# Kernel tuning notes

Hardware: AMD Instinct MI355X
Metric: run time of the kernel (lower is better)

The kernel has to match this reference:

```python
import jax, jax.numpy as jnp
import numpy as np

B, D, H, G = 16384, 512, 128, 18  # batch, input_dim, hidden_dim, num_genres

def setup_inputs() -> dict:
    key = jax.random.key(0)
    ks = jax.random.split(key, 12)
    s = lambda *sh: 1.0 / np.sqrt(sh[-2] if len(sh) > 1 else 1.0)
    item_features = jax.random.normal(ks[0], (B, D), dtype=jnp.float32)
    genre_vectors = jax.random.randint(ks[1], (B, G), 0, 2).astype(jnp.float32)  # multi-hot
    # stacked per-genre expert MLP params: D -> 2H -> H -> H
    W1 = jax.random.normal(ks[2], (G, D, 2 * H), dtype=jnp.float32) / np.sqrt(D)
    b1 = jnp.zeros((G, 2 * H), dtype=jnp.float32)
    W2 = jax.random.normal(ks[3], (G, 2 * H, H), dtype=jnp.float32) / np.sqrt(2 * H)
    b2 = jnp.zeros((G, H), dtype=jnp.float32)
    W3 = jax.random.normal(ks[4], (G, H, H), dtype=jnp.float32) / np.sqrt(H)
    b3 = jnp.zeros((G, H), dtype=jnp.float32)
    # genre attention: D -> G, softmax
    Wa = jax.random.normal(ks[5], (D, G), dtype=jnp.float32) / np.sqrt(D)
    ba = jnp.zeros((G,), dtype=jnp.float32)
    # aggregation: (D + H) -> D
    Wagg = jax.random.normal(ks[6], (D + H, D), dtype=jnp.float32) / np.sqrt(D + H)
    bagg = jnp.zeros((D,), dtype=jnp.float32)
    return dict(item_features=item_features, genre_vectors=genre_vectors,
                W1=W1, b1=b1, W2=W2, b2=b2, W3=W3, b3=b3,
                Wa=Wa, ba=ba, Wagg=Wagg, bagg=bagg)

def reference(item_features, genre_vectors, W1, b1, W2, b2, W3, b3, Wa, ba, Wagg, bagg):
    # genre attention weights [B, G]
    attn = jax.nn.softmax(item_features @ Wa + ba, axis=-1)
    # run every genre expert on every item (dense grouped GEMM), then mask.
    h1 = jax.nn.relu(jnp.einsum('bd,gdh->bgh', item_features, W1) + b1)   # [B,G,2H]
    h2 = jax.nn.relu(jnp.einsum('bgh,ghk->bgk', h1, W2) + b2)            # [B,G,H]
    h3 = jnp.einsum('bgk,gkm->bgm', h2, W3) + b3                          # [B,G,H]
    # per (item, genre) weight: attention * membership, zero where not a member
    w = jnp.where(genre_vectors > 0, attn * genre_vectors, 0.0)          # [B,G]
    refinements = jnp.einsum('bg,bgm->bm', w, h3)                         # [B,H]
    combined = jnp.concatenate([item_features, refinements], axis=-1)    # [B,D+H]
    return jax.nn.relu(combined @ Wagg + bagg)                            # [B,D]
```

## Files before the change

kernel.cpp:

```cpp
#include <hip/hip_runtime.h>

#define NB 16384
#define ND 512
#define NH 128
#define NHH 256
#define NG 18

typedef short s8v __attribute__((ext_vector_type(8)));
typedef __bf16 bf8v __attribute__((ext_vector_type(8)));
typedef float f16v __attribute__((ext_vector_type(16)));
typedef unsigned int u4v __attribute__((ext_vector_type(4)));

static __device__ __forceinline__ unsigned short f2bf(float f) {
  unsigned int u = __builtin_bit_cast(unsigned int, f);
  u += 0x7FFFu + ((u >> 16) & 1u);
  return (unsigned short)(u >> 16);
}

static __device__ __forceinline__ f16v mfma32(s8v a, s8v b, f16v c) {
  return __builtin_amdgcn_mfma_f32_32x32x16_bf16(
      __builtin_bit_cast(bf8v, a), __builtin_bit_cast(bf8v, b), c, 0, 0, 0);
}

static __device__ __forceinline__ f16v zf16() {
  f16v v;
#pragma unroll
  for (int i = 0; i < 16; ++i) v[i] = 0.f;
  return v;
}

__global__ __launch_bounds__(256) void k_pack(const float* __restrict__ in,
                                              unsigned short* __restrict__ out,
                                              int K, int N) {
  const int g = blockIdx.y;
  const int c = blockIdx.x * 256 + threadIdx.x;
  const int nk = K >> 4;
  const int l = c & 63;
  const int t = c >> 6;
  const int nt = t / nk;
  const int ks = t - nt * nk;
  const int k0 = (ks << 4) + ((l >> 5) << 3);
  const int col = (nt << 5) + (l & 31);
  const float* ip = in + (size_t)g * K * N + (size_t)k0 * N + col;
  u4v pk;
#pragma unroll
  for (int j = 0; j < 4; ++j) {
    float x0 = ip[(size_t)(2 * j) * N];
    float x1 = ip[(size_t)(2 * j + 1) * N];
    pk[j] = (unsigned)f2bf(x0) | ((unsigned)f2bf(x1) << 16);
  }
  *(u4v*)(out + (size_t)g * K * N + ((size_t)c << 3)) = pk;
}

__global__ __launch_bounds__(256) void k_wat(const float* __restrict__ wa,
                                             float* __restrict__ wat) {
  int tid = blockIdx.x * 256 + threadIdx.x;
  if (tid < NG * ND) {
    int g = tid >> 9, d = tid & (ND - 1);
    wat[tid] = wa[d * NG + g];
  }
}

__global__ __launch_bounds__(256) void k_attn(const float* __restrict__ X,
                                              const float* __restrict__ GV,
                                              const float* __restrict__ wat,
                                              const float* __restrict__ ba,
                                              float* __restrict__ w,
                                              unsigned short* __restrict__ xb) {
  __shared__ float wl[NG * ND];
  const int tid = threadIdx.x;
  for (int i = tid; i < NG * ND; i += 256) wl[i] = wat[i];
  __syncthreads();
  const int lane = tid & 63;
  const int row = (blockIdx.x << 2) + (tid >> 6);
  const float* xr = X + (size_t)row * ND + (lane << 3);
  float x[8];
  {
    float4 a = *(const float4*)xr;
    float4 b = *(const float4*)(xr + 4);
    x[0] = a.x; x[1] = a.y; x[2] = a.z; x[3] = a.w;
    x[4] = b.x; x[5] = b.y; x[6] = b.z; x[7] = b.w;
  }
  {
    u4v p;
#pragma unroll
    for (int j = 0; j < 4; ++j)
      p[j] = (unsigned)f2bf(x[2 * j]) | ((unsigned)f2bf(x[2 * j + 1]) << 16);
    *(u4v*)(xb + (size_t)row * ND + (lane << 3)) = p;
  }
  float lg[NG];
#pragma unroll
  for (int g = 0; g < NG; ++g) {
    const float* wr = wl + g * ND + (lane << 3);
    float s = 0.f;
#pragma unroll
    for (int j = 0; j < 8; ++j) s += x[j] * wr[j];
    lg[g] = s;
  }
#pragma unroll
  for (int off = 32; off > 0; off >>= 1) {
#pragma unroll
    for (int g = 0; g < NG; ++g) lg[g] += __shfl_xor(lg[g], off);
  }
  float m = -3.4e38f;
#pragma unroll
  for (int g = 0; g < NG; ++g) { lg[g] += ba[g]; m = fmaxf(m, lg[g]); }
  float s = 0.f;
#pragma unroll
  for (int g = 0; g < NG; ++g) { lg[g] = expf(lg[g] - m); s += lg[g]; }
  float inv = 1.f / s;
  if (lane < NG) {
    float gv = GV[(size_t)row * NG + lane];
    w[(size_t)row * NG + lane] = gv > 0.f ? lg[lane] * inv * gv : 0.f;
  }
}

__global__ __launch_bounds__(512, 2) void k_main(
    const unsigned short* __restrict__ xb,
    const float* __restrict__ wbg,
    const unsigned short* __restrict__ w1p,
    const unsigned short* __restrict__ w2p,
    const unsigned short* __restrict__ w3p,
    const unsigned short* __restrict__ w4p,
    const float* __restrict__ b1, const float* __restrict__ b2,
    const float* __restrict__ b3, const float* __restrict__ bagg,
    float* __restrict__ out) {
  __shared__ __align__(16) char smem[119808];
  char* const XT = smem;
  char* const H1 = smem + 65536;
  char* const H2 = smem + 98304;
  float* const WL = (float*)(smem + 114688);

  const int tid = threadIdx.x;
  const int row0 = blockIdx.x << 6;
  const int wid = tid >> 6, lane = tid & 63;
  const int l31 = lane & 31, lh = lane >> 5;

#pragma unroll
  for (int i = 0; i < 8; ++i) {
    int ck = (i << 9) + tid;
    int mt = ck >> 11, ks = (ck >> 6) & 31, l = ck & 63;
    int grow = row0 + (mt << 5) + (l & 31);
    int col8 = (ks << 1) + (l >> 5);
    *(u4v*)(XT + (ck << 4)) =
        *(const u4v*)(xb + ((size_t)grow << 9) + (col8 << 3));
  }
  for (int i = tid; i < 64 * NG; i += 512) {
    int r = i / NG, g = i - r * NG;
    WL[r * 20 + g] = wbg[(size_t)(row0 + r) * NG + g];
  }

  const int nt2 = wid & 3, mt2 = wid >> 2;
  const unsigned short* const bp1 = w1p + (wid << 14) + (lane << 3);
  const unsigned short* const bp2 = w2p + (nt2 << 13) + (lane << 3);
  const unsigned short* const bp3 = w3p + (nt2 << 12) + (lane << 3);
  const unsigned short* const bp4a = w4p + (size_t)wid * 20480 + (lane << 3);
  const unsigned short* const bp4b = w4p + (size_t)(wid + 8) * 20480 + (lane << 3);

  s8v bq[4];
#pragma unroll
  for (int i = 0; i < 4; ++i) bq[i] = *(const s8v*)(bp1 + (i << 9));

  f16v racc = zf16();
  __syncthreads();

  for (int g = 0; g < NG; ++g) {
    const unsigned short* const bp1g = bp1 + (size_t)g * 131072;
    f16v acc1[2][2];
    acc1[0][0] = zf16(); acc1[0][1] = zf16();
    acc1[1][0] = zf16(); acc1[1][1] = zf16();
#pragma unroll
    for (int ks = 0; ks < 32; ++ks) {
      s8v bn;
      const bool havenext = (ks < 28) || (g + 1 < NG);
      if (havenext) {
        size_t off = (ks < 28) ? (size_t)((ks + 4) << 9)
                               : (size_t)131072 + ((ks - 28) << 9);
        bn = *(const s8v*)(bp1g + off);
      }
      s8v a0 = *(const s8v*)(XT + (ks << 10) + (lane << 4));
      s8v a1 = *(const s8v*)(XT + 32768 + (ks << 10) + (lane << 4));
      acc1[0][ks & 1] = mfma32(a0, bq[ks & 3], acc1[0][ks & 1]);
      acc1[1][ks & 1] = mfma32(a1, bq[ks & 3], acc1[1][ks & 1]);
      if (havenext) bq[ks & 3] = bn;
    }
    {
      const float bv1 = b1[(g << 8) + (wid << 5) + l31];
      const int gcol = (wid << 5) + l31;
      const int cbase = ((gcol >> 4) << 10) + ((((gcol >> 3) & 1) << 5) << 4) +
                        ((gcol & 7) << 1);
#pragma unroll
      for (int mt = 0; mt < 2; ++mt)
#pragma unroll
        for (int r = 0; r < 16; ++r) {
          const int rl = (r & 3) + ((r >> 2) << 3) + (lh << 2);
          float v = fmaxf(acc1[mt][0][r] + acc1[mt][1][r] + bv1, 0.f);
          *(unsigned short*)(H1 + (mt << 14) + cbase + (rl << 4)) = f2bf(v);
        }
    }
    const unsigned short* const bp2g = bp2 + ((size_t)g << 15);
    s8v b2f[16];
#pragma unroll
    for (int ks = 0; ks < 16; ++ks) b2f[ks] = *(const s8v*)(bp2g + (ks << 9));
    const float bv2 = b2[(g << 7) + (nt2 << 5) + l31];
    __syncthreads();

    f16v acc2a = zf16(), acc2b = zf16();
#pragma unroll
    for (int ks = 0; ks < 16; ks += 2) {
      s8v a0 = *(const s8v*)(H1 + (mt2 << 14) + (ks << 10) + (lane << 4));
      s8v a1 = *(const s8v*)(H1 + (mt2 << 14) + ((ks + 1) << 10) + (lane << 4));
      acc2a = mfma32(a0, b2f[ks], acc2a);
      acc2b = mfma32(a1, b2f[ks + 1], acc2b);
    }
    {
      const int gcol = (nt2 << 5) + l31;
      const int cbase = ((gcol >> 4) << 10) + ((((gcol >> 3) & 1) << 5) << 4) +
                        ((gcol & 7) << 1);
#pragma unroll
      for (int r = 0; r < 16; ++r) {
        const int rl = (r & 3) + ((r >> 2) << 3) + (lh << 2);
        float v = fmaxf(acc2a[r] + acc2b[r] + bv2, 0.f);
        *(unsigned short*)(H2 + (mt2 << 13) + cbase + (rl << 4)) = f2bf(v);
      }
    }
    const unsigned short* const bp3g = bp3 + ((size_t)g << 14);
    s8v b3f[8];
#pragma unroll
    for (int ks = 0; ks < 8; ++ks) b3f[ks] = *(const s8v*)(bp3g + (ks << 9));
    const float bv3 = b3[(g << 7) + (nt2 << 5) + l31];
    __syncthreads();

    f16v acc3a = zf16(), acc3b = zf16();
#pragma unroll
    for (int ks = 0; ks < 8; ks += 2) {
      s8v a0 = *(const s8v*)(H2 + (mt2 << 13) + (ks << 10) + (lane << 4));
      s8v a1 = *(const s8v*)(H2 + (mt2 << 13) + ((ks + 1) << 10) + (lane << 4));
      acc3a = mfma32(a0, b3f[ks], acc3a);
      acc3b = mfma32(a1, b3f[ks + 1], acc3b);
    }
#pragma unroll
    for (int r = 0; r < 16; ++r) {
      const int rl = (r & 3) + ((r >> 2) << 3) + (lh << 2);
      const int grow = (mt2 << 5) + rl;
      racc[r] += WL[grow * 20 + g] * (acc3a[r] + acc3b[r] + bv3);
    }
  }

  s8v bq4[2][2];
#pragma unroll
  for (int k = 0; k < 2; ++k) {
    bq4[k][0] = *(const s8v*)(bp4a + (k << 9));
    bq4[k][1] = *(const s8v*)(bp4b + (k << 9));
  }
  __syncthreads();
  {
    const int gcol = (nt2 << 5) + l31;
    const int cbase = ((gcol >> 4) << 10) + ((((gcol >> 3) & 1) << 5) << 4) +
                      ((gcol & 7) << 1);
#pragma unroll
    for (int r = 0; r < 16; ++r) {
      const int rl = (r & 3) + ((r >> 2) << 3) + (lh << 2);
      *(unsigned short*)(H2 + (mt2 << 13) + cbase + (rl << 4)) = f2bf(racc[r]);
    }
  }
  __syncthreads();

  f16v acc4[2][2];
  acc4[0][0] = zf16(); acc4[0][1] = zf16();
  acc4[1][0] = zf16(); acc4[1][1] = zf16();
#pragma unroll
  for (int ks = 0; ks < 40; ++ks) {
    s8v bn0, bn1;
    if (ks < 38) {
      bn0 = *(const s8v*)(bp4a + ((ks + 2) << 9));
      bn1 = *(const s8v*)(bp4b + ((ks + 2) << 9));
    }
    s8v a0, a1;
    if (ks < 32) {
      a0 = *(const s8v*)(XT + (ks << 10) + (lane << 4));
      a1 = *(const s8v*)(XT + 32768 + (ks << 10) + (lane << 4));
    } else {
      a0 = *(const s8v*)(H2 + ((ks - 32) << 10) + (lane << 4));
      a1 = *(const s8v*)(H2 + 8192 + ((ks - 32) << 10) + (lane << 4));
    }
    acc4[0][0] = mfma32(a0, bq4[ks & 1][0], acc4[0][0]);
    acc4[1][0] = mfma32(a1, bq4[ks & 1][0], acc4[1][0]);
    acc4[0][1] = mfma32(a0, bq4[ks & 1][1], acc4[0][1]);
    acc4[1][1] = mfma32(a1, bq4[ks & 1][1], acc4[1][1]);
    if (ks < 38) { bq4[ks & 1][0] = bn0; bq4[ks & 1][1] = bn1; }
  }
  {
    const float bv4a = bagg[(wid << 5) + l31];
    const float bv4b = bagg[((wid + 8) << 5) + l31];
#pragma unroll
    for (int mt = 0; mt < 2; ++mt)
#pragma unroll
      for (int r = 0; r < 16; ++r) {
        const int rl = (r & 3) + ((r >> 2) << 3) + (lh << 2);
        const size_t rbase = (size_t)(row0 + (mt << 5) + rl) << 9;
        out[rbase + (wid << 5) + l31] = fmaxf(acc4[mt][0][r] + bv4a, 0.f);
        out[rbase + ((wid + 8) << 5) + l31] = fmaxf(acc4[mt][1][r] + bv4b, 0.f);
      }
  }
}

#define OFF_W     0u
#define OFF_XB    1179648u
#define OFF_W1P   17956864u
#define OFF_W2P   22675456u
#define OFF_W3P   23855104u
#define OFF_W4P   24444928u
#define OFF_WAT   25100288u

extern "C" void kernel_launch(void* const* d_in, const int* in_sizes, int n_in,
                              void* d_out, int out_size, void* d_ws, size_t ws_size,
                              hipStream_t stream) {
  const float* X    = (const float*)d_in[0];
  const float* GV   = (const float*)d_in[1];
  const float* W1   = (const float*)d_in[2];
  const float* b1   = (const float*)d_in[3];
  const float* W2   = (const float*)d_in[4];
  const float* b2   = (const float*)d_in[5];
  const float* W3   = (const float*)d_in[6];
  const float* b3   = (const float*)d_in[7];
  const float* Wa   = (const float*)d_in[8];
  const float* ba   = (const float*)d_in[9];
  const float* Wagg = (const float*)d_in[10];
  const float* bagg = (const float*)d_in[11];
  float* out = (float*)d_out;
  char* ws = (char*)d_ws;

  float* w_ws           = (float*)(ws + OFF_W);
  unsigned short* xb    = (unsigned short*)(ws + OFF_XB);
  unsigned short* w1p   = (unsigned short*)(ws + OFF_W1P);
  unsigned short* w2p   = (unsigned short*)(ws + OFF_W2P);
  unsigned short* w3p   = (unsigned short*)(ws + OFF_W3P);
  unsigned short* w4p   = (unsigned short*)(ws + OFF_W4P);
  float* wat            = (float*)(ws + OFF_WAT);

  k_pack<<<dim3(64, 18), 256, 0, stream>>>(W1, w1p, 512, 256);
  k_pack<<<dim3(16, 18), 256, 0, stream>>>(W2, w2p, 256, 128);
  k_pack<<<dim3(8, 18), 256, 0, stream>>>(W3, w3p, 128, 128);
  k_pack<<<dim3(160, 1), 256, 0, stream>>>(Wagg, w4p, 640, 512);
  k_wat<<<36, 256, 0, stream>>>(Wa, wat);
  k_attn<<<4096, 256, 0, stream>>>(X, GV, wat, ba, w_ws, xb);
  k_main<<<256, 512, 0, stream>>>(xb, w_ws, w1p, w2p, w3p, w4p,
                                  b1, b2, b3, bagg, out);
}
```

Before: 196.8 us.

## Retile layer-1 GEMM per wave and XOR-swizzle hidden activation LDS layout

Layer 1 now gives each wave one M-tile and two N-tiles instead of two M-tiles and one N-tile. Each wave reads one A fragment from LDS and streams two weight column tiles, which changes the ratio of LDS reads to global weight loads. The H1, H2 and refinement stores and loads to shared memory now use XOR swizzle masks, meant to reduce LDS bank conflicts on the scattered bf16 epilogue writes. The cost is doubled per-wave global weight traffic in layer 1 and some extra index arithmetic.

```diff
diff --git a/kernel.cpp b/kernel.cpp
--- a/kernel.cpp
+++ b/kernel.cpp
@@ -28,6 +28,8 @@
   for (int i = 0; i < 16; ++i) v[i] = 0.f;
   return v;
 }
+
+#define KM(ks) (((((ks) & 1) << 5)) | ((((ks) >> 1) & 1) << 6))
 
 __global__ __launch_bounds__(256) void k_pack(const float* __restrict__ in,
                                               unsigned short* __restrict__ out,
@@ -135,6 +137,7 @@
   const int row0 = blockIdx.x << 6;
   const int wid = tid >> 6, lane = tid & 63;
   const int l31 = lane & 31, lh = lane >> 5;
+  const int lb = (lane << 4) ^ (lh << 4);
 
 #pragma unroll
   for (int i = 0; i < 8; ++i) {
@@ -150,92 +153,101 @@
     WL[r * 20 + g] = wbg[(size_t)(row0 + r) * NG + g];
   }
 
+  const int mt1 = wid >> 2;
+  const int ntp = (wid & 3) << 1;
   const int nt2 = wid & 3, mt2 = wid >> 2;
-  const unsigned short* const bp1 = w1p + (wid << 14) + (lane << 3);
+
+  const unsigned short* const bp1A = w1p + (ntp << 14) + (lane << 3);
+  const unsigned short* const bp1B = w1p + ((ntp + 1) << 14) + (lane << 3);
   const unsigned short* const bp2 = w2p + (nt2 << 13) + (lane << 3);
   const unsigned short* const bp3 = w3p + (nt2 << 12) + (lane << 3);
   const unsigned short* const bp4a = w4p + (size_t)wid * 20480 + (lane << 3);
   const unsigned short* const bp4b = w4p + (size_t)(wid + 8) * 20480 + (lane << 3);
 
-  s8v bq[4];
-#pragma unroll
-  for (int i = 0; i < 4; ++i) bq[i] = *(const s8v*)(bp1 + (i << 9));
+  const int gcA = (ntp << 5) + l31;
+  const int gcB = gcA + 32;
+  const int gc2 = (nt2 << 5) + l31;
+  const int cbA = ((gcA >> 4) << 10) + (((gcA >> 3) & 1) << 9) + ((gcA & 7) << 1);
+  const int cbB = ((gcB >> 4) << 10) + (((gcB >> 3) & 1) << 9) + ((gcB & 7) << 1);
+  const int cb2 = ((gc2 >> 4) << 10) + (((gc2 >> 3) & 1) << 9) + ((gc2 & 7) << 1);
+  const int mA = (((cbA >> 9) & 1) << 4) | (((cbA >> 10) & 1) << 5) | (((cbA >> 11) & 1) << 6);
+  const int mB = (((cbB >> 9) & 1) << 4) | (((cbB >> 10) & 1) << 5) | (((cbB >> 11) & 1) << 6);
+  const int m2 = (((cb2 >> 9) & 1) << 4) | (((cb2 >> 10) & 1) << 5) | (((cb2 >> 11) & 1) << 6);
+
+  s8v bqA[4], bqB[4];
+#pragma unroll
+  for (int i = 0; i < 4; ++i) {
+    bqA[i] = *(const s8v*)(bp1A + (i << 9));
+    bqB[i] = *(const s8v*)(bp1B + (i << 9));
+  }
 
   f16v racc = zf16();
   __syncthreads();
 
   for (int g = 0; g < NG; ++g) {
-    const unsigned short* const bp1g = bp1 + (size_t)g * 131072;
-    f16v acc1[2][2];
-    acc1[0][0] = zf16(); acc1[0][1] = zf16();
-    acc1[1][0] = zf16(); acc1[1][1] = zf16();
+    const unsigned short* const bp1Ag = bp1A + (size_t)g * 131072;
+    const unsigned short* const bp1Bg = bp1B + (size_t)g * 131072;
+    f16v accA = zf16(), accB = zf16();
 #pragma unroll
     for (int ks = 0; ks < 32; ++ks) {
-      s8v bn;
+      s8v bnA, bnB;
       const bool havenext = (ks < 28) || (g + 1 < NG);
       if (havenext) {
         size_t off = (ks < 28) ? (size_t)((ks + 4) << 9)
                                : (size_t)131072 + ((ks - 28) << 9);
-        bn = *(const s8v*)(bp1g + off);
+        bnA = *(const s8v*)(bp1Ag + off);
+        bnB = *(const s8v*)(bp1Bg + off);
       }
-      s8v a0 = *(const s8v*)(XT + (ks << 10) + (lane << 4));
-      s8v a1 = *(const s8v*)(XT + 32768 + (ks << 10) + (lane << 4));
-      acc1[0][ks & 1] = mfma32(a0, bq[ks & 3], acc1[0][ks & 1]);
-      acc1[1][ks & 1] = mfma32(a1, bq[ks & 3], acc1[1][ks & 1]);
-      if (havenext) bq[ks & 3] = bn;
+      s8v a = *(const s8v*)(XT + (mt1 << 15) + (ks << 10) + (lane << 4));
+      accA = mfma32(a, bqA[ks & 3], accA);
+      accB = mfma32(a, bqB[ks & 3], accB);
+      if (havenext) { bqA[ks & 3] = bnA; bqB[ks & 3] = bnB; }
     }
     {
-      const float bv1 = b1[(g << 8) + (wid << 5) + l31];
-      const int gcol = (wid << 5) + l31;
-      const int cbase = ((gcol >> 4) << 10) + ((((gcol >> 3) & 1) << 5) << 4) +
-                        ((gcol & 7) << 1);
-#pragma unroll
-      for (int mt = 0; mt < 2; ++mt)
-#pragma unroll
-        for (int r = 0; r < 16; ++r) {
-          const int rl = (r & 3) + ((r >> 2) << 3) + (lh << 2);
-          float v = fmaxf(acc1[mt][0][r] + acc1[mt][1][r] + bv1, 0.f);
-          *(unsigned short*)(H1 + (mt << 14) + cbase + (rl << 4)) = f2bf(v);
-        }
+      const float bv1a = b1[(g << 8) + gcA];
+      const float bv1b = b1[(g << 8) + gcB];
+#pragma unroll
+      for (int r = 0; r < 16; ++r) {
+        const int rl = (r & 3) + ((r >> 2) << 3) + (lh << 2);
+        float vA = fmaxf(accA[r] + bv1a, 0.f);
+        float vB = fmaxf(accB[r] + bv1b, 0.f);
+        *(unsigned short*)(H1 + (mt1 << 14) + ((cbA + (rl << 4)) ^ mA)) = f2bf(vA);
+        *(unsigned short*)(H1 + (mt1 << 14) + ((cbB + (rl << 4)) ^ mB)) = f2bf(vB);
+      }
     }
     const unsigned short* const bp2g = bp2 + ((size_t)g << 15);
     s8v b2f[16];
 #pragma unroll
     for (int ks = 0; ks < 16; ++ks) b2f[ks] = *(const s8v*)(bp2g + (ks << 9));
-    const float bv2 = b2[(g << 7) + (nt2 << 5) + l31];
+    const float bv2 = b2[(g << 7) + gc2];
     __syncthreads();
 
     f16v acc2a = zf16(), acc2b = zf16();
 #pragma unroll
     for (int ks = 0; ks < 16; ks += 2) {
-      s8v a0 = *(const s8v*)(H1 + (mt2 << 14) + (ks << 10) + (lane << 4));
-      s8v a1 = *(const s8v*)(H1 + (mt2 << 14) + ((ks + 1) << 10) + (lane << 4));
+      s8v a0 = *(const s8v*)(H1 + (mt2 << 14) + (((ks << 10) + lb) ^ KM(ks)));
+      s8v a1 = *(const s8v*)(H1 + (mt2 << 14) + ((((ks + 1) << 10) + lb) ^ KM(ks + 1)));
       acc2a = mfma32(a0, b2f[ks], acc2a);
       acc2b = mfma32(a1, b2f[ks + 1], acc2b);
     }
-    {
-      const int gcol = (nt2 << 5) + l31;
-      const int cbase = ((gcol >> 4) << 10) + ((((gcol >> 3) & 1) << 5) << 4) +
-                        ((gcol & 7) << 1);
-#pragma unroll
-      for (int r = 0; r < 16; ++r) {
-        const int rl = (r & 3) + ((r >> 2) << 3) + (lh << 2);
-        float v = fmaxf(acc2a[r] + acc2b[r] + bv2, 0.f);
-        *(unsigned short*)(H2 + (mt2 << 13) + cbase + (rl << 4)) = f2bf(v);
-      }
+#pragma unroll
+    for (int r = 0; r < 16; ++r) {
+      const int rl = (r & 3) + ((r >> 2) << 3) + (lh << 2);
+      float v = fmaxf(acc2a[r] + acc2b[r] + bv2, 0.f);
+      *(unsigned short*)(H2 + (mt2 << 13) + ((cb2 + (rl << 4)) ^ m2)) = f2bf(v);
     }
     const unsigned short* const bp3g = bp3 + ((size_t)g << 14);
     s8v b3f[8];
 #pragma unroll
     for (int ks = 0; ks < 8; ++ks) b3f[ks] = *(const s8v*)(bp3g + (ks << 9));
-    const float bv3 = b3[(g << 7) + (nt2 << 5) + l31];
+    const float bv3 = b3[(g << 7) + gc2];
     __syncthreads();
 
     f16v acc3a = zf16(), acc3b = zf16();
 #pragma unroll
     for (int ks = 0; ks < 8; ks += 2) {
-      s8v a0 = *(const s8v*)(H2 + (mt2 << 13) + (ks << 10) + (lane << 4));
-      s8v a1 = *(const s8v*)(H2 + (mt2 << 13) + ((ks + 1) << 10) + (lane << 4));
+      s8v a0 = *(const s8v*)(H2 + (mt2 << 13) + (((ks << 10) + lb) ^ KM(ks)));
+      s8v a1 = *(const s8v*)(H2 + (mt2 << 13) + ((((ks + 1) << 10) + lb) ^ KM(ks + 1)));
       acc3a = mfma32(a0, b3f[ks], acc3a);
       acc3b = mfma32(a1, b3f[ks + 1], acc3b);
     }
@@ -254,15 +266,10 @@
     bq4[k][1] = *(const s8v*)(bp4b + (k << 9));
   }
   __syncthreads();
-  {
-    const int gcol = (nt2 << 5) + l31;
-    const int cbase = ((gcol >> 4) << 10) + ((((gcol >> 3) & 1) << 5) << 4) +
-                      ((gcol & 7) << 1);
-#pragma unroll
-    for (int r = 0; r < 16; ++r) {
-      const int rl = (r & 3) + ((r >> 2) << 3) + (lh << 2);
-      *(unsigned short*)(H2 + (mt2 << 13) + cbase + (rl << 4)) = f2bf(racc[r]);
-    }
+#pragma unroll
+  for (int r = 0; r < 16; ++r) {
+    const int rl = (r & 3) + ((r >> 2) << 3) + (lh << 2);
+    *(unsigned short*)(H2 + (mt2 << 13) + ((cb2 + (rl << 4)) ^ m2)) = f2bf(racc[r]);
   }
   __syncthreads();
 
@@ -281,8 +288,9 @@
       a0 = *(const s8v*)(XT + (ks << 10) + (lane << 4));
       a1 = *(const s8v*)(XT + 32768 + (ks << 10) + (lane << 4));
     } else {
-      a0 = *(const s8v*)(H2 + ((ks - 32) << 10) + (lane << 4));
-      a1 = *(const s8v*)(H2 + 8192 + ((ks - 32) << 10) + (lane << 4));
+      const int hk = ks - 32;
+      a0 = *(const s8v*)(H2 + (((hk << 10) + lb) ^ KM(hk)));
+      a1 = *(const s8v*)(H2 + 8192 + (((hk << 10) + lb) ^ KM(hk)));
     }
     acc4[0][0] = mfma32(a0, bq4[ks & 1][0], acc4[0][0]);
     acc4[1][0] = mfma32(a1, bq4[ks & 1][0], acc4[1][0]);
```

Measured after the change: 202.1 us. +2.7%, slower.
